# Performance work log

Hardware: AMD Instinct MI355X
Metric: run time of the kernel (lower is better)

## Reference

```python
import jax, jax.numpy as jnp
import numpy as np
from jax import lax

# pywt db4 decomposition lowpass filter
_DEC_LO_NP = np.array([-0.010597401784997278, 0.032883011666982945,
                        0.030841381835986965, -0.18703481171888114,
                        -0.02798376941698385, 0.6308807679295904,
                        0.7148465705525415, 0.23037781330885523], dtype=np.float32)
_SIGNS = np.array([(-1.0) ** (k + 1) for k in range(8)], dtype=np.float32)
DEC_LO = jnp.asarray(_DEC_LO_NP)                    # dec_lo
DEC_HI = jnp.asarray(_DEC_LO_NP[::-1] * _SIGNS)     # dec_hi (QMF)
LF = 8
MAX_LEVEL = 4
# analysis kernels: torch cross-correlates with reversed dec filters == true conv
H_ANA = jnp.stack([DEC_LO[::-1], DEC_HI[::-1]])[:, None, :]  # (2,1,LF)
# synthesis: torch conv_transpose with rec filters == xcorr(dilated x, flip(rec)) = xcorr with dec
G0F = DEC_LO[None, None, :]
G1F = DEC_HI[None, None, :]
DN = ('NCH', 'OIH', 'NCH')


def _dwt_step(x):
    # x: (N, Lx) -> (lo, hi) each (N, outsize); pytorch_wavelets afb1d, mode='symmetric'
    N = x.shape[-1]
    outsize = (N + LF - 1) // 2          # pywt.dwt_coeff_len
    p = 2 * (outsize - 1) - N + LF
    xp = jnp.pad(x, ((0, 0), (p // 2, (p + 1) // 2)), mode='symmetric')
    y = lax.conv_general_dilated(xp[:, None, :], H_ANA, (2,), 'VALID',
                                 dimension_numbers=DN)  # (N,2,outsize)
    return y[:, 0, :], y[:, 1, :]


def _idwt_step(lo, hi):
    # pytorch_wavelets sfb1d: conv_transpose(stride=2, padding=LF-2)
    # == lhs-dilated xcorr with flipped rec filters (= dec filters), pad 1 each side
    y0 = lax.conv_general_dilated(lo[:, None, :], G0F, (1,), [(1, 1)],
                                  lhs_dilation=(2,), dimension_numbers=DN)
    y1 = lax.conv_general_dilated(hi[:, None, :], G1F, (1,), [(1, 1)],
                                  lhs_dilation=(2,), dimension_numbers=DN)
    return (y0 + y1)[:, 0, :]            # (N, 2*Llo + 2 - LF)


def dywpe(x, proj_w, proj_b, scale_emb, gate_w, gate_b):
    B, L, _ = x.shape
    d_model = scale_emb.shape[1]
    # channel_proj -> mono signal (B, L)
    x_mono = (jnp.einsum('blc,oc->blo', x, proj_w) + proj_b)[..., 0]
    # multi-level DWT
    lo = x_mono
    highs = []
    for _ in range(MAX_LEVEL):
        lo, hi = _dwt_step(lo)
        highs.append(hi)
    # gates: sigmoid(g) * tanh(v), per scale -> (MAX_LEVEL+1, d_model)
    gated = scale_emb @ gate_w.T + gate_b
    g, v = jnp.split(gated, 2, axis=-1)
    gates = jax.nn.sigmoid(g) * jnp.tanh(v)

    def mod(coef, gate):  # (B,Lc) x (d,) -> (B*d, Lc): outer product, fold d into batch
        return (coef[:, None, :] * gate[None, :, None]).reshape(B * d_model, -1)

    x0 = mod(lo, gates[0])
    hs = [mod(highs[i], gates[i + 1]) for i in range(MAX_LEVEL)]
    # IDWT, coarsest level first
    for h in hs[::-1]:
        if x0.shape[-1] > h.shape[-1]:
            x0 = x0[:, :h.shape[-1]]
        x0 = _idwt_step(x0, h)
    pe = x0.reshape(B, d_model, -1).transpose(0, 2, 1)  # (B, L', d_model)
    if pe.shape[1] < L:
        pe = jnp.pad(pe, ((0, 0), (0, L - pe.shape[1]), (0, 0)))
    elif pe.shape[1] > L:
        pe = pe[:, :L]
    return pe


def setup_inputs() -> dict:
    key = jax.random.key(0)
    ks = jax.random.split(key, 6)
    B, L, d_x, d_model, J = 32, 4096, 8, 512, 4
    return {
        'x': jax.random.normal(ks[0], (B, L, d_x), dtype=jnp.float32),
        'proj_w': jax.random.normal(ks[1], (1, d_x), dtype=jnp.float32) * 0.3,
        'proj_b': jax.random.normal(ks[2], (1,), dtype=jnp.float32) * 0.02,
        'scale_emb': jax.random.normal(ks[3], (J + 1, d_model), dtype=jnp.float32),
        'gate_w': jax.random.normal(ks[4], (2 * d_model, d_model), dtype=jnp.float32) * 0.04,
        'gate_b': jax.random.normal(ks[5], (2 * d_model,), dtype=jnp.float32) * 0.02,
    }


def reference(x, proj_w, proj_b, scale_emb, gate_w, gate_b):
    return dywpe(x, proj_w, proj_b, scale_emb, gate_w, gate_b)
```

## Files before the change

kernel.cpp:

```cpp
#include <hip/hip_runtime.h>

#define NB    32
#define LSEQ  4096
#define DM    512
#define ROWS  64
#define CHUNKS (LSEQ / ROWS)

typedef float f32x4 __attribute__((ext_vector_type(4)));

__device__ __constant__ float c_DL[8] = {
    -0.010597401784997278f,  0.032883011666982945f,  0.030841381835986965f,
    -0.18703481171888114f,  -0.02798376941698385f,   0.6308807679295904f,
     0.7148465705525415f,    0.23037781330885523f};
__device__ __constant__ float c_DH[8] = {
    -0.23037781330885523f,   0.7148465705525415f,   -0.6308807679295904f,
    -0.02798376941698385f,   0.18703481171888114f,   0.030841381835986965f,
    -0.032883011666982945f, -0.010597401784997278f};

__device__ __forceinline__ int imin(int a, int b) { return a < b ? a : b; }
__device__ __forceinline__ int imax(int a, int b) { return a > b ? a : b; }

__device__ __forceinline__ int reflect_idx(int i, int N) {
    if (i < 0)  i = -1 - i;
    if (i >= N) i = 2 * N - 1 - i;
    return i;
}

template <bool HI>
__device__ void fwd_range(const float* __restrict__ src, int src_lo, int Nsrc,
                          float* __restrict__ dst, int d_lo, int d_hi) {
    for (int t = d_lo + (int)threadIdx.x; t <= d_hi; t += 256) {
        int base = 2 * t - 6;
        float acc = 0.f;
#pragma unroll
        for (int k = 0; k < 8; ++k) {
            float xv = src[reflect_idx(base + k, Nsrc) - src_lo];
            acc = fmaf(xv, HI ? c_DH[7 - k] : c_DL[7 - k], acc);
        }
        dst[t - d_lo] = acc;
    }
}

template <bool HI>
__device__ void inv_range(const float* __restrict__ c, int c_lo,
                          float* __restrict__ y, int y_lo, int y_hi) {
    for (int t = y_lo + (int)threadIdx.x; t <= y_hi; t += 256) {
        int base = (t >> 1) - c_lo;
        int odd = t & 1;
        float f0 = odd ? (HI ? c_DH[0] : c_DL[0]) : (HI ? c_DH[1] : c_DL[1]);
        float f1 = odd ? (HI ? c_DH[2] : c_DL[2]) : (HI ? c_DH[3] : c_DL[3]);
        float f2 = odd ? (HI ? c_DH[4] : c_DL[4]) : (HI ? c_DH[5] : c_DL[5]);
        float f3 = odd ? (HI ? c_DH[6] : c_DL[6]) : (HI ? c_DH[7] : c_DL[7]);
        float acc = c[base] * f0;
        acc = fmaf(c[base + 1], f1, acc);
        acc = fmaf(c[base + 2], f2, acc);
        acc = fmaf(c[base + 3], f3, acc);
        y[t - y_lo] = acc;
    }
}

__global__ __launch_bounds__(1024) void gates_kernel(
    const float* __restrict__ scale_emb, const float* __restrict__ gate_w,
    const float* __restrict__ gate_b, float* __restrict__ gates) {
    int lane = threadIdx.x & 63;
    int c = blockIdx.x * 16 + (threadIdx.x >> 6);
    const float4* rg = (const float4*)(gate_w + (size_t)c * DM) + lane * 2;
    const float4* rv = (const float4*)(gate_w + (size_t)(c + DM) * DM) + lane * 2;
    float4 a0 = rg[0], a1 = rg[1];
    float4 b0 = rv[0], b1 = rv[1];
    float gacc[5], vacc[5];
#pragma unroll
    for (int j = 0; j < 5; ++j) {
        const float4* sj = (const float4*)(scale_emb + (size_t)j * DM) + lane * 2;
        float4 s0 = sj[0], s1 = sj[1];
        float ga;
        ga = s0.x * a0.x;            ga = fmaf(s0.y, a0.y, ga);
        ga = fmaf(s0.z, a0.z, ga);   ga = fmaf(s0.w, a0.w, ga);
        ga = fmaf(s1.x, a1.x, ga);   ga = fmaf(s1.y, a1.y, ga);
        ga = fmaf(s1.z, a1.z, ga);   ga = fmaf(s1.w, a1.w, ga);
        float va;
        va = s0.x * b0.x;            va = fmaf(s0.y, b0.y, va);
        va = fmaf(s0.z, b0.z, va);   va = fmaf(s0.w, b0.w, va);
        va = fmaf(s1.x, b1.x, va);   va = fmaf(s1.y, b1.y, va);
        va = fmaf(s1.z, b1.z, va);   va = fmaf(s1.w, b1.w, va);
        gacc[j] = ga;
        vacc[j] = va;
    }
#pragma unroll
    for (int j = 0; j < 5; ++j) {
#pragma unroll
        for (int off = 32; off > 0; off >>= 1) {
            gacc[j] += __shfl_xor(gacc[j], off, 64);
            vacc[j] += __shfl_xor(vacc[j], off, 64);
        }
    }
    if (lane == 0) {
        float bg = gate_b[c], bv = gate_b[DM + c];
#pragma unroll
        for (int j = 0; j < 5; ++j) {
            float g = gacc[j] + bg;
            float v = vacc[j] + bv;
            float sg = 1.f / (1.f + expf(-g));
            gates[j * DM + c] = sg * tanhf(v);
        }
    }
}

__global__ __launch_bounds__(256, 8) void fused_kernel(
    const float* __restrict__ x, const float* __restrict__ proj_w,
    const float* __restrict__ proj_b, const float* __restrict__ gates,
    float* __restrict__ out) {
    __shared__ float GL[5 * DM];
    __shared__ float XW[288];
    __shared__ float LO1[140], LO2[68], LO3[32];
    __shared__ float HI1[36], H2W[24], H3W[16], L4W[12], H4W[12];
    __shared__ float AW[16], A4W[16], A3W[24], BW[24], B4W[24];
    __shared__ float P0W[36], P2W[36], P3W[36], P4W[36];
    __shared__ float SJ[5 * ROWS];

    int bid = blockIdx.x;
    int b  = bid >> 6;
    int l0 = (bid & 63) * ROWS;

    int p0 = l0 >> 1,  p1 = ((l0 + ROWS - 1) >> 1) + 3;
    int b0 = p0 >> 1,  b1 = (p1 >> 1) + 3;
    int a0 = b0 >> 1,  a1 = (b1 >> 1) + 3;
    int w0 = a0 >> 1,  w1 = (a1 >> 1) + 3;
    int t3lo = imax(imin(imin(2 * w0 - 6, a0), 517), 0);
    int t3hi = imin(imax(imax(2 * w1 + 1, a1), 0), 517);
    int t2lo = imax(imin(2 * t3lo - 6, 2 * a0 - 6), 0);
    int t2hi = imin(imax(2 * t3hi + 1, 2 * a1 + 1), 1028);
    int t1lo = imax(imin(2 * t2lo - 6, 2 * b0 - 6), 0);
    int t1hi = imin(imax(2 * t2hi + 1, 2 * b1 + 1), 2050);
    int txlo = imax(imin(2 * t1lo - 6, 2 * p0 - 6), 0);
    int txhi = imin(imax(2 * t1hi + 1, 2 * p1 + 1), 4095);

    for (int i = threadIdx.x; i < 5 * DM / 4; i += 256)
        ((f32x4*)GL)[i] = ((const f32x4*)gates)[i];
    float w[8];
#pragma unroll
    for (int k = 0; k < 8; ++k) w[k] = proj_w[k];
    float pb = proj_b[0];
    const float* xb = x + (size_t)b * LSEQ * 8;
    for (int i = txlo + (int)threadIdx.x; i <= txhi; i += 256) {
        const float4* xv = (const float4*)(xb + (size_t)i * 8);
        float4 q0 = xv[0], q1 = xv[1];
        float acc = pb;
        acc = fmaf(q0.x, w[0], acc); acc = fmaf(q0.y, w[1], acc);
        acc = fmaf(q0.z, w[2], acc); acc = fmaf(q0.w, w[3], acc);
        acc = fmaf(q1.x, w[4], acc); acc = fmaf(q1.y, w[5], acc);
        acc = fmaf(q1.z, w[6], acc); acc = fmaf(q1.w, w[7], acc);
        XW[i - txlo] = acc;
    }
    __syncthreads();

    fwd_range<false>(XW, txlo, 4096, LO1, t1lo, t1hi);
    fwd_range<true >(XW, txlo, 4096, HI1, p0, p1);
    __syncthreads();
    fwd_range<false>(LO1, t1lo, 2051, LO2, t2lo, t2hi);
    fwd_range<true >(LO1, t1lo, 2051, H2W, b0, b1);
    __syncthreads();
    fwd_range<false>(LO2, t2lo, 1029, LO3, t3lo, t3hi);
    fwd_range<true >(LO2, t2lo, 1029, H3W, a0, a1);
    __syncthreads();
    fwd_range<false>(LO3, t3lo, 518, L4W, w0, w1);
    fwd_range<true >(LO3, t3lo, 518, H4W, w0, w1);
    __syncthreads();

    inv_range<false>(L4W, w0, AW,  a0, a1);
    inv_range<true >(H4W, w0, A4W, a0, a1);
    inv_range<true >(H3W, a0, A3W, b0, b1);
    inv_range<true >(H2W, b0, P2W, p0, p1);
    __syncthreads();
    inv_range<false>(AW,  a0, BW,  b0, b1);
    inv_range<false>(A4W, a0, B4W, b0, b1);
    inv_range<false>(A3W, b0, P3W, p0, p1);
    __syncthreads();
    inv_range<false>(BW,  b0, P0W, p0, p1);
    inv_range<false>(B4W, b0, P4W, p0, p1);
    __syncthreads();

    for (int idx = threadIdx.x; idx < 5 * ROWS; idx += 256) {
        int j = idx >> 6;
        int r = idx & (ROWS - 1);
        int l = l0 + r;
        int base = (l >> 1) - p0;
        int odd = l & 1;
        const float* Pj = (j == 0) ? P0W : (j == 1) ? HI1 :
                          (j == 2) ? P2W : (j == 3) ? P3W : P4W;
        bool hi = (j == 1);
        float f0 = odd ? (hi ? c_DH[0] : c_DL[0]) : (hi ? c_DH[1] : c_DL[1]);
        float f1 = odd ? (hi ? c_DH[2] : c_DL[2]) : (hi ? c_DH[3] : c_DL[3]);
        float f2 = odd ? (hi ? c_DH[4] : c_DL[4]) : (hi ? c_DH[5] : c_DL[5]);
        float f3 = odd ? (hi ? c_DH[6] : c_DL[6]) : (hi ? c_DH[7] : c_DL[7]);
        float acc = Pj[base] * f0;
        acc = fmaf(Pj[base + 1], f1, acc);
        acc = fmaf(Pj[base + 2], f2, acc);
        acc = fmaf(Pj[base + 3], f3, acc);
        SJ[idx] = acc;
    }
    __syncthreads();

    int half = threadIdx.x >> 7;
    int c4 = threadIdx.x & 127;
    f32x4 g0 = ((const f32x4*)(GL + 0 * DM))[c4];
    f32x4 g1 = ((const f32x4*)(GL + 1 * DM))[c4];
    f32x4 g2 = ((const f32x4*)(GL + 2 * DM))[c4];
    f32x4 g3 = ((const f32x4*)(GL + 3 * DM))[c4];
    f32x4 g4 = ((const f32x4*)(GL + 4 * DM))[c4];

    size_t rowbase = (size_t)b * LSEQ + l0;
#pragma unroll 4
    for (int r = 0; r < ROWS / 2; ++r) {
        int rr = r * 2 + half;
        float s0 = SJ[rr];
        float s1 = SJ[64 + rr];
        float s2 = SJ[128 + rr];
        float s3 = SJ[192 + rr];
        float s4 = SJ[256 + rr];
        f32x4 acc;
        acc.x = fmaf(s4, g4.x, fmaf(s3, g3.x, fmaf(s2, g2.x, fmaf(s1, g1.x, s0 * g0.x))));
        acc.y = fmaf(s4, g4.y, fmaf(s3, g3.y, fmaf(s2, g2.y, fmaf(s1, g1.y, s0 * g0.y))));
        acc.z = fmaf(s4, g4.z, fmaf(s3, g3.z, fmaf(s2, g2.z, fmaf(s1, g1.z, s0 * g0.z))));
        acc.w = fmaf(s4, g4.w, fmaf(s3, g3.w, fmaf(s2, g2.w, fmaf(s1, g1.w, s0 * g0.w))));
        __builtin_nontemporal_store(acc, (f32x4*)out + (rowbase + rr) * (DM / 4) + c4);
    }
}

extern "C" void kernel_launch(void* const* d_in, const int* in_sizes, int n_in,
                              void* d_out, int out_size, void* d_ws, size_t ws_size,
                              hipStream_t stream) {
    const float* x         = (const float*)d_in[0];
    const float* proj_w    = (const float*)d_in[1];
    const float* proj_b    = (const float*)d_in[2];
    const float* scale_emb = (const float*)d_in[3];
    const float* gate_w    = (const float*)d_in[4];
    const float* gate_b    = (const float*)d_in[5];
    float* out   = (float*)d_out;
    float* gates = (float*)d_ws;

    gates_kernel<<<32, 1024, 0, stream>>>(scale_emb, gate_w, gate_b, gates);
    fused_kernel<<<NB * CHUNKS, 256, 0, stream>>>(x, proj_w, proj_b, gates, out);
}
```

Measured before the change: 64.90 us.

## Split fused kernel into basis and expand kernels via workspace

Splits the fused kernel into two launches. A basis kernel computes the five per-row wavelet basis values and writes them to global workspace, and a separate expand kernel multiplies them by the gates and streams the large output with finer-grained blocks of 32 rows. The aim is to decouple the latency-bound wavelet stage from the bandwidth-bound output write and raise parallelism in the store phase. In exchange it adds an extra kernel launch and a global round trip for the intermediate basis array.

Result: slower. 70.55 us (+8.7%).

```diff
diff --git a/kernel.cpp b/kernel.cpp
--- a/kernel.cpp
+++ b/kernel.cpp
@@ -7,6 +7,9 @@
 #define CHUNKS (LSEQ / ROWS)
 
 typedef float f32x4 __attribute__((ext_vector_type(4)));
+
+#define GATES_OFF 0
+#define S_OFF     (5 * DM)
 
 __device__ __constant__ float c_DL[8] = {
     -0.010597401784997278f,  0.032883011666982945f,  0.030841381835986965f,
@@ -106,17 +109,14 @@
     }
 }
 
-__global__ __launch_bounds__(256, 8) void fused_kernel(
+__global__ __launch_bounds__(256) void basis_kernel(
     const float* __restrict__ x, const float* __restrict__ proj_w,
-    const float* __restrict__ proj_b, const float* __restrict__ gates,
-    float* __restrict__ out) {
-    __shared__ float GL[5 * DM];
+    const float* __restrict__ proj_b, float* __restrict__ S) {
     __shared__ float XW[288];
     __shared__ float LO1[140], LO2[68], LO3[32];
     __shared__ float HI1[36], H2W[24], H3W[16], L4W[12], H4W[12];
     __shared__ float AW[16], A4W[16], A3W[24], BW[24], B4W[24];
     __shared__ float P0W[36], P2W[36], P3W[36], P4W[36];
-    __shared__ float SJ[5 * ROWS];
 
     int bid = blockIdx.x;
     int b  = bid >> 6;
@@ -135,8 +135,6 @@
     int txlo = imax(imin(2 * t1lo - 6, 2 * p0 - 6), 0);
     int txhi = imin(imax(2 * t1hi + 1, 2 * p1 + 1), 4095);
 
-    for (int i = threadIdx.x; i < 5 * DM / 4; i += 256)
-        ((f32x4*)GL)[i] = ((const f32x4*)gates)[i];
     float w[8];
 #pragma unroll
     for (int k = 0; k < 8; ++k) w[k] = proj_w[k];
@@ -197,33 +195,43 @@
         acc = fmaf(Pj[base + 1], f1, acc);
         acc = fmaf(Pj[base + 2], f2, acc);
         acc = fmaf(Pj[base + 3], f3, acc);
-        SJ[idx] = acc;
-    }
-    __syncthreads();
-
+        S[(size_t)j * (NB * LSEQ) + (size_t)b * LSEQ + l] = acc;
+    }
+}
+
+__global__ __launch_bounds__(256) void expand_kernel(
+    const float* __restrict__ ws, float* __restrict__ out) {
+    const float* S = ws + S_OFF;
+    const float* gates = ws + GATES_OFF;
+    __shared__ float gl[5 * DM];
+    for (int i = threadIdx.x; i < 5 * DM / 4; i += 256)
+        ((f32x4*)gl)[i] = ((const f32x4*)gates)[i];
+    __syncthreads();
+
+    const size_t BL = (size_t)NB * LSEQ;
     int half = threadIdx.x >> 7;
     int c4 = threadIdx.x & 127;
-    f32x4 g0 = ((const f32x4*)(GL + 0 * DM))[c4];
-    f32x4 g1 = ((const f32x4*)(GL + 1 * DM))[c4];
-    f32x4 g2 = ((const f32x4*)(GL + 2 * DM))[c4];
-    f32x4 g3 = ((const f32x4*)(GL + 3 * DM))[c4];
-    f32x4 g4 = ((const f32x4*)(GL + 4 * DM))[c4];
-
-    size_t rowbase = (size_t)b * LSEQ + l0;
+    f32x4 g0 = ((const f32x4*)(gl + 0 * DM))[c4];
+    f32x4 g1 = ((const f32x4*)(gl + 1 * DM))[c4];
+    f32x4 g2 = ((const f32x4*)(gl + 2 * DM))[c4];
+    f32x4 g3 = ((const f32x4*)(gl + 3 * DM))[c4];
+    f32x4 g4 = ((const f32x4*)(gl + 4 * DM))[c4];
+
+    int rowBase = blockIdx.x * 32;
 #pragma unroll 4
-    for (int r = 0; r < ROWS / 2; ++r) {
-        int rr = r * 2 + half;
-        float s0 = SJ[rr];
-        float s1 = SJ[64 + rr];
-        float s2 = SJ[128 + rr];
-        float s3 = SJ[192 + rr];
-        float s4 = SJ[256 + rr];
+    for (int r = 0; r < 16; ++r) {
+        int row = rowBase + r * 2 + half;
+        float s0 = S[row];
+        float s1 = S[BL + row];
+        float s2 = S[2 * BL + row];
+        float s3 = S[3 * BL + row];
+        float s4 = S[4 * BL + row];
         f32x4 acc;
         acc.x = fmaf(s4, g4.x, fmaf(s3, g3.x, fmaf(s2, g2.x, fmaf(s1, g1.x, s0 * g0.x))));
         acc.y = fmaf(s4, g4.y, fmaf(s3, g3.y, fmaf(s2, g2.y, fmaf(s1, g1.y, s0 * g0.y))));
         acc.z = fmaf(s4, g4.z, fmaf(s3, g3.z, fmaf(s2, g2.z, fmaf(s1, g1.z, s0 * g0.z))));
         acc.w = fmaf(s4, g4.w, fmaf(s3, g3.w, fmaf(s2, g2.w, fmaf(s1, g1.w, s0 * g0.w))));
-        __builtin_nontemporal_store(acc, (f32x4*)out + (rowbase + rr) * (DM / 4) + c4);
+        __builtin_nontemporal_store(acc, (f32x4*)out + (size_t)row * (DM / 4) + c4);
     }
 }
 
@@ -236,9 +244,10 @@
     const float* scale_emb = (const float*)d_in[3];
     const float* gate_w    = (const float*)d_in[4];
     const float* gate_b    = (const float*)d_in[5];
-    float* out   = (float*)d_out;
-    float* gates = (float*)d_ws;
-
-    gates_kernel<<<32, 1024, 0, stream>>>(scale_emb, gate_w, gate_b, gates);
-    fused_kernel<<<NB * CHUNKS, 256, 0, stream>>>(x, proj_w, proj_b, gates, out);
-}
+    float* out = (float*)d_out;
+    float* ws  = (float*)d_ws;
+
+    gates_kernel<<<32, 1024, 0, stream>>>(scale_emb, gate_w, gate_b, ws + GATES_OFF);
+    basis_kernel<<<NB * CHUNKS, 256, 0, stream>>>(x, proj_w, proj_b, ws + S_OFF);
+    expand_kernel<<<(NB * LSEQ) / 32, 256, 0, stream>>>(ws, out);
+}
```

## Warp-specialize wavelet prologue onto one wave and drop block barriers

Applied to the files above, without the earlier changes.

Wave 0 now runs the channel projection, all forward DWT levels and the partial inverse transforms alone, with lane-strided loops. The other three waves copy the gate table into shared memory at the same time. This removes eight block-wide __syncthreads between small stages and overlaps the gate load with the wavelet work. Correctness relies on LDS accesses from a single wavefront staying in program order. The launch-bounds occupancy hint also drops from 8 to 4 blocks per CU.

Result: slower. 67.96 us (+4.7%).

```diff
diff --git a/kernel.cpp b/kernel.cpp
--- a/kernel.cpp
+++ b/kernel.cpp
@@ -27,9 +27,9 @@
 }
 
 template <bool HI>
-__device__ void fwd_range(const float* __restrict__ src, int src_lo, int Nsrc,
-                          float* __restrict__ dst, int d_lo, int d_hi) {
-    for (int t = d_lo + (int)threadIdx.x; t <= d_hi; t += 256) {
+__device__ void fwd_range_w(const float* __restrict__ src, int src_lo, int Nsrc,
+                            float* __restrict__ dst, int d_lo, int d_hi, int lane) {
+    for (int t = d_lo + lane; t <= d_hi; t += 64) {
         int base = 2 * t - 6;
         float acc = 0.f;
 #pragma unroll
@@ -42,9 +42,9 @@
 }
 
 template <bool HI>
-__device__ void inv_range(const float* __restrict__ c, int c_lo,
-                          float* __restrict__ y, int y_lo, int y_hi) {
-    for (int t = y_lo + (int)threadIdx.x; t <= y_hi; t += 256) {
+__device__ void inv_range_w(const float* __restrict__ c, int c_lo,
+                            float* __restrict__ y, int y_lo, int y_hi, int lane) {
+    for (int t = y_lo + lane; t <= y_hi; t += 64) {
         int base = (t >> 1) - c_lo;
         int odd = t & 1;
         float f0 = odd ? (HI ? c_DH[0] : c_DL[0]) : (HI ? c_DH[1] : c_DL[1]);
@@ -106,7 +106,7 @@
     }
 }
 
-__global__ __launch_bounds__(256, 8) void fused_kernel(
+__global__ __launch_bounds__(256, 4) void fused_kernel(
     const float* __restrict__ x, const float* __restrict__ proj_w,
     const float* __restrict__ proj_b, const float* __restrict__ gates,
     float* __restrict__ out) {
@@ -135,49 +135,46 @@
     int txlo = imax(imin(2 * t1lo - 6, 2 * p0 - 6), 0);
     int txhi = imin(imax(2 * t1hi + 1, 2 * p1 + 1), 4095);
 
-    for (int i = threadIdx.x; i < 5 * DM / 4; i += 256)
-        ((f32x4*)GL)[i] = ((const f32x4*)gates)[i];
-    float w[8];
-#pragma unroll
-    for (int k = 0; k < 8; ++k) w[k] = proj_w[k];
-    float pb = proj_b[0];
-    const float* xb = x + (size_t)b * LSEQ * 8;
-    for (int i = txlo + (int)threadIdx.x; i <= txhi; i += 256) {
-        const float4* xv = (const float4*)(xb + (size_t)i * 8);
-        float4 q0 = xv[0], q1 = xv[1];
-        float acc = pb;
-        acc = fmaf(q0.x, w[0], acc); acc = fmaf(q0.y, w[1], acc);
-        acc = fmaf(q0.z, w[2], acc); acc = fmaf(q0.w, w[3], acc);
-        acc = fmaf(q1.x, w[4], acc); acc = fmaf(q1.y, w[5], acc);
-        acc = fmaf(q1.z, w[6], acc); acc = fmaf(q1.w, w[7], acc);
-        XW[i - txlo] = acc;
-    }
-    __syncthreads();
-
-    fwd_range<false>(XW, txlo, 4096, LO1, t1lo, t1hi);
-    fwd_range<true >(XW, txlo, 4096, HI1, p0, p1);
-    __syncthreads();
-    fwd_range<false>(LO1, t1lo, 2051, LO2, t2lo, t2hi);
-    fwd_range<true >(LO1, t1lo, 2051, H2W, b0, b1);
-    __syncthreads();
-    fwd_range<false>(LO2, t2lo, 1029, LO3, t3lo, t3hi);
-    fwd_range<true >(LO2, t2lo, 1029, H3W, a0, a1);
-    __syncthreads();
-    fwd_range<false>(LO3, t3lo, 518, L4W, w0, w1);
-    fwd_range<true >(LO3, t3lo, 518, H4W, w0, w1);
-    __syncthreads();
-
-    inv_range<false>(L4W, w0, AW,  a0, a1);
-    inv_range<true >(H4W, w0, A4W, a0, a1);
-    inv_range<true >(H3W, a0, A3W, b0, b1);
-    inv_range<true >(H2W, b0, P2W, p0, p1);
-    __syncthreads();
-    inv_range<false>(AW,  a0, BW,  b0, b1);
-    inv_range<false>(A4W, a0, B4W, b0, b1);
-    inv_range<false>(A3W, b0, P3W, p0, p1);
-    __syncthreads();
-    inv_range<false>(BW,  b0, P0W, p0, p1);
-    inv_range<false>(B4W, b0, P4W, p0, p1);
+    int wid = threadIdx.x >> 6;
+    int lane = threadIdx.x & 63;
+
+    if (wid != 0) {
+        for (int i = (threadIdx.x - 64); i < 5 * DM / 4; i += 192)
+            ((f32x4*)GL)[i] = ((const f32x4*)gates)[i];
+    } else {
+        float w[8];
+#pragma unroll
+        for (int k = 0; k < 8; ++k) w[k] = proj_w[k];
+        float pb = proj_b[0];
+        const float* xb = x + (size_t)b * LSEQ * 8;
+        for (int i = txlo + lane; i <= txhi; i += 64) {
+            const float4* xv = (const float4*)(xb + (size_t)i * 8);
+            float4 q0 = xv[0], q1 = xv[1];
+            float acc = pb;
+            acc = fmaf(q0.x, w[0], acc); acc = fmaf(q0.y, w[1], acc);
+            acc = fmaf(q0.z, w[2], acc); acc = fmaf(q0.w, w[3], acc);
+            acc = fmaf(q1.x, w[4], acc); acc = fmaf(q1.y, w[5], acc);
+            acc = fmaf(q1.z, w[6], acc); acc = fmaf(q1.w, w[7], acc);
+            XW[i - txlo] = acc;
+        }
+        fwd_range_w<false>(XW, txlo, 4096, LO1, t1lo, t1hi, lane);
+        fwd_range_w<true >(XW, txlo, 4096, HI1, p0, p1, lane);
+        fwd_range_w<false>(LO1, t1lo, 2051, LO2, t2lo, t2hi, lane);
+        fwd_range_w<true >(LO1, t1lo, 2051, H2W, b0, b1, lane);
+        fwd_range_w<false>(LO2, t2lo, 1029, LO3, t3lo, t3hi, lane);
+        fwd_range_w<true >(LO2, t2lo, 1029, H3W, a0, a1, lane);
+        fwd_range_w<false>(LO3, t3lo, 518, L4W, w0, w1, lane);
+        fwd_range_w<true >(LO3, t3lo, 518, H4W, w0, w1, lane);
+        inv_range_w<false>(L4W, w0, AW,  a0, a1, lane);
+        inv_range_w<true >(H4W, w0, A4W, a0, a1, lane);
+        inv_range_w<true >(H3W, a0, A3W, b0, b1, lane);
+        inv_range_w<true >(H2W, b0, P2W, p0, p1, lane);
+        inv_range_w<false>(AW,  a0, BW,  b0, b1, lane);
+        inv_range_w<false>(A4W, a0, B4W, b0, b1, lane);
+        inv_range_w<false>(A3W, b0, P3W, p0, p1, lane);
+        inv_range_w<false>(BW,  b0, P0W, p0, p1, lane);
+        inv_range_w<false>(B4W, b0, P4W, p0, p1, lane);
+    }
     __syncthreads();
 
     for (int idx = threadIdx.x; idx < 5 * ROWS; idx += 256) {
```
